# Optimization experiments

Hardware: AMD Instinct MI355X
Metric: run time of the kernel (lower is better)

The kernel has to match this reference:

```python
import jax, jax.numpy as jnp
import numpy as np

NUM_HEADS = 16
HEAD_SIZE = 64
N_EMBD = 1024
BLOCK_SIZE = 2048
BATCH = 2


def setup_inputs() -> dict:
    key = jax.random.key(0)
    ks = jax.random.split(key, 6)
    s = 0.02
    x = jax.random.normal(ks[0], (BATCH, BLOCK_SIZE, N_EMBD), dtype=jnp.float32)
    Wq = jax.random.normal(ks[1], (NUM_HEADS, N_EMBD, HEAD_SIZE), dtype=jnp.float32) * s
    Wk = jax.random.normal(ks[2], (NUM_HEADS, N_EMBD, HEAD_SIZE), dtype=jnp.float32) * s
    Wv = jax.random.normal(ks[3], (NUM_HEADS, N_EMBD, HEAD_SIZE), dtype=jnp.float32) * s
    Wproj = jax.random.normal(ks[4], (NUM_HEADS * HEAD_SIZE, N_EMBD), dtype=jnp.float32) * s
    bproj = jax.random.normal(ks[5], (N_EMBD,), dtype=jnp.float32) * s
    return {"x": x, "Wq": Wq, "Wk": Wk, "Wv": Wv, "Wproj": Wproj, "bproj": bproj}


def reference(x, Wq, Wk, Wv, Wproj, bproj):
    B, S, E = x.shape
    H, _, D = Wq.shape
    # batched per-head projections (equivalent to the per-head Linear loop)
    q = jnp.einsum('bse,hed->bhsd', x, Wq)
    k = jnp.einsum('bse,hed->bhsd', x, Wk)
    v = jnp.einsum('bse,hed->bhsd', x, Wv)
    scale = D ** -0.5
    scores = jnp.einsum('bhqd,bhkd->bhqk', q, k) * scale
    causal = jnp.tril(jnp.ones((S, S), dtype=bool))
    scores = jnp.where(causal, scores, jnp.finfo(scores.dtype).min)
    attn = jax.nn.softmax(scores, axis=-1)
    out = jnp.einsum('bhqk,bhkd->bhqd', attn, v)  # [B,H,S,D]
    out = out.transpose(0, 2, 1, 3).reshape(B, S, H * D)  # concat heads
    return out @ Wproj + bproj
```

## Files before the change

kernel.cpp:

```cpp
#include <hip/hip_runtime.h>
#include <hip/hip_fp16.h>

#define BATCH 2
#define SEQ 2048
#define EMB 1024
#define NH 16
#define HDIM 64

typedef _Float16 h16;
typedef __attribute__((ext_vector_type(8))) _Float16 h8;
typedef __attribute__((ext_vector_type(4))) _Float16 h4;
typedef __attribute__((ext_vector_type(2))) _Float16 h2;
typedef __attribute__((ext_vector_type(4))) float f32x4;

#define MFMA16(a, b, c) __builtin_amdgcn_mfma_f32_16x16x32_f16((a), (b), (c), 0, 0, 0)

__device__ __forceinline__ void g2l16(const void* g, void* l) {
    __builtin_amdgcn_global_load_lds(
        (const __attribute__((address_space(1))) unsigned int*)g,
        (__attribute__((address_space(3))) unsigned int*)l, 16, 0, 0);
}

__global__ __launch_bounds__(256) void k_cast_x(const float* __restrict__ x,
                                                h16* __restrict__ xh) {
    int i = (blockIdx.x * 256 + threadIdx.x) * 4;
    float4 v = *(const float4*)(x + i);
    h4 o = { (h16)v.x, (h16)v.y, (h16)v.z, (h16)v.w };
    *(h4*)(xh + i) = o;
}

__global__ __launch_bounds__(256) void k_tr_qkv3(const float* __restrict__ wq,
                                                 const float* __restrict__ wk,
                                                 const float* __restrict__ wv,
                                                 h16* __restrict__ wcat) {
    __shared__ h16 ld[64][65];
    int g = blockIdx.x >> 4;
    int t = blockIdx.x & 15;
    int h = g / 3, mat = g - h * 3;
    const float* src = (mat == 0) ? wq : (mat == 1) ? wk : wv;
    int e0 = t * 64;
    int c0 = threadIdx.x & 63, r0 = threadIdx.x >> 6;
#pragma unroll
    for (int i = 0; i < 16; i++) {
        int e = i * 4 + r0;
        ld[c0][e] = (h16)src[((size_t)((h << 10) | (e0 + e))) * 64 + c0];
    }
    __syncthreads();
#pragma unroll
    for (int i = 0; i < 16; i++) {
        int d = i * 4 + r0;
        wcat[((size_t)(g * 64 + d) << 10) | (e0 + c0)] = ld[d][c0];
    }
}

__global__ __launch_bounds__(256) void k_tr_wp(const float* __restrict__ w,
                                               h16* __restrict__ wt) {
    __shared__ h16 ld[64][65];
    int kt = blockIdx.x & 15, ntl = blockIdx.x >> 4;
    int c0 = threadIdx.x & 63, r0 = threadIdx.x >> 6;
#pragma unroll
    for (int i = 0; i < 16; i++) {
        int k = i * 4 + r0;
        ld[c0][k] = (h16)w[((size_t)(kt * 64 + k) << 10) | (ntl * 64 + c0)];
    }
    __syncthreads();
#pragma unroll
    for (int i = 0; i < 16; i++) {
        int n = i * 4 + r0;
        wt[((size_t)(ntl * 64 + n) << 10) | (kt * 64 + c0)] = ld[n][c0];
    }
}

__global__ __launch_bounds__(256) void k_qkv(
    const h16* __restrict__ xh, const h16* __restrict__ wcat,
    h16* __restrict__ Q, h16* __restrict__ Kk, h16* __restrict__ Vt) {
    __shared__ h16 As[128 * 64];
    __shared__ h16 Bs[128 * 64];
    int tid = threadIdx.x;
    int wave = tid >> 6, lane = tid & 63;
    int lr = lane & 15, lg = lane >> 4, lx = lr & 7;
    int wr = wave >> 1, wc = wave & 1;
    int swz = (blockIdx.x & 7) * 96 + (blockIdx.x >> 3);
    int nt = swz % 24, mt = swz / 24;

    const char* Ab = (const char*)xh + (size_t)mt * 128 * 2048;
    const char* Bb = (const char*)wcat + (size_t)nt * 128 * 2048;
    int rl = lane >> 3, gc = lane & 7;
    size_t lofs = (size_t)rl * 2048 + ((gc ^ rl) << 4);

    f32x4 acc[4][4];
#pragma unroll
    for (int m = 0; m < 4; m++)
#pragma unroll
        for (int n = 0; n < 4; n++) acc[m][n] = (f32x4){0.f, 0.f, 0.f, 0.f};

    for (int k0 = 0; k0 < 1024; k0 += 64) {
        size_t kb = (size_t)k0 * 2;
#pragma unroll
        for (int c = 0; c < 4; c++) {
            int rb = c * 32 + wave * 8;
            g2l16(Ab + (size_t)rb * 2048 + lofs + kb, As + rb * 64);
            g2l16(Bb + (size_t)rb * 2048 + lofs + kb, Bs + rb * 64);
        }
        __syncthreads();
#pragma unroll
        for (int dc = 0; dc < 2; dc++) {
            h8 a[4], b[4];
#pragma unroll
            for (int m = 0; m < 4; m++)
                a[m] = *(const h8*)&As[(wr * 64 + m * 16 + lr) * 64 + (((dc * 4 + lg) ^ lx) << 3)];
#pragma unroll
            for (int n = 0; n < 4; n++)
                b[n] = *(const h8*)&Bs[(wc * 64 + n * 16 + lr) * 64 + (((dc * 4 + lg) ^ lx) << 3)];
#pragma unroll
            for (int m = 0; m < 4; m++)
#pragma unroll
                for (int n = 0; n < 4; n++)
                    acc[m][n] = MFMA16(a[m], b[n], acc[m][n]);
        }
        __syncthreads();
    }

    int g = nt * 2 + wc;
    int mat = g % 3, hh = g / 3;
    int row0 = mt * 128 + wr * 64;
    if (mat == 2) {
#pragma unroll
        for (int m = 0; m < 4; m++)
#pragma unroll
            for (int n = 0; n < 4; n++) {
                int row = row0 + m * 16 + lg * 4;
                int b = row >> 11, s = row & 2047;
                int bh = b * 16 + hh;
                int d = n * 16 + lr;
                h4 o = { (h16)acc[m][n][0], (h16)acc[m][n][1],
                         (h16)acc[m][n][2], (h16)acc[m][n][3] };
                *(h4*)&Vt[((size_t)bh * 64 + d) * 2048 + s] = o;
            }
    } else {
        h16* dst = mat ? Kk : Q;
        float qs = mat ? 1.0f : 0.18033688011112042f;
#pragma unroll
        for (int m = 0; m < 4; m++)
#pragma unroll
            for (int n = 0; n < 4; n++)
#pragma unroll
                for (int r = 0; r < 4; r++) {
                    int row = row0 + m * 16 + lg * 4 + r;
                    int bh = (row >> 11) * 16 + hh, s = row & 2047;
                    dst[((size_t)bh * 2048 + s) * 64 + n * 16 + lr] =
                        (h16)(acc[m][n][r] * qs);
                }
    }
}

__global__ __launch_bounds__(256) void k_proj(
    const h16* __restrict__ att, const h16* __restrict__ wpt,
    const float* __restrict__ bias, float* __restrict__ out) {
    __shared__ h16 As[128 * 64];
    __shared__ h16 Bs[64 * 64];
    int tid = threadIdx.x;
    int wave = tid >> 6, lane = tid & 63;
    int lr = lane & 15, lg = lane >> 4, lx = lr & 7;
    int swz = (blockIdx.x & 7) * 64 + (blockIdx.x >> 3);
    int nt = swz & 15, mt = swz >> 4;

    const char* Ab = (const char*)att + (size_t)mt * 128 * 2048;
    const char* Bb = (const char*)wpt + (size_t)nt * 64 * 2048;
    int rl = lane >> 3, gc = lane & 7;
    size_t lofs = (size_t)rl * 2048 + ((gc ^ rl) << 4);

    f32x4 acc[2][4];
#pragma unroll
    for (int m = 0; m < 2; m++)
#pragma unroll
        for (int n = 0; n < 4; n++) acc[m][n] = (f32x4){0.f, 0.f, 0.f, 0.f};

    for (int k0 = 0; k0 < 1024; k0 += 64) {
        size_t kb = (size_t)k0 * 2;
#pragma unroll
        for (int c = 0; c < 4; c++) {
            int rb = c * 32 + wave * 8;
            g2l16(Ab + (size_t)rb * 2048 + lofs + kb, As + rb * 64);
            if (c < 2)
                g2l16(Bb + (size_t)rb * 2048 + lofs + kb, Bs + rb * 64);
        }
        __syncthreads();
#pragma unroll
        for (int dc = 0; dc < 2; dc++) {
            h8 a[2], b[4];
#pragma unroll
            for (int m = 0; m < 2; m++)
                a[m] = *(const h8*)&As[(wave * 32 + m * 16 + lr) * 64 + (((dc * 4 + lg) ^ lx) << 3)];
#pragma unroll
            for (int n = 0; n < 4; n++)
                b[n] = *(const h8*)&Bs[(n * 16 + lr) * 64 + (((dc * 4 + lg) ^ lx) << 3)];
#pragma unroll
            for (int m = 0; m < 2; m++)
#pragma unroll
                for (int n = 0; n < 4; n++)
                    acc[m][n] = MFMA16(a[m], b[n], acc[m][n]);
        }
        __syncthreads();
    }

#pragma unroll
    for (int m = 0; m < 2; m++)
#pragma unroll
        for (int n = 0; n < 4; n++)
#pragma unroll
            for (int r = 0; r < 4; r++) {
                int row = mt * 128 + wave * 32 + m * 16 + lg * 4 + r;
                int col = nt * 64 + n * 16 + lr;
                out[(size_t)row * 1024 + col] = acc[m][n][r] + bias[col];
            }
}

__device__ __forceinline__ void stage_kv(h16* Kb, h16* Vb,
                                         const h16* Kp, const h16* Vp,
                                         int ks0, int wave, int lane) {
    int rl = lane >> 3, gc = lane & 7;
    int sg = gc ^ rl;
#pragma unroll
    for (int c8 = 0; c8 < 2; c8++) {
        int rb = wave * 16 + c8 * 8;
        int row = rb + rl;
        g2l16((const char*)Kp + ((size_t)(ks0 + row) << 7) + (sg << 4), Kb + rb * 64);
        g2l16((const char*)Vp + ((size_t)row << 12) + ((size_t)ks0 << 1) + (sg << 4), Vb + rb * 64);
    }
}

__global__ __launch_bounds__(256, 4) void k_attn(
    const h16* __restrict__ Q, const h16* __restrict__ Kk,
    const h16* __restrict__ Vt, h16* __restrict__ att) {
    __shared__ h16 Kb[2][64 * 64];
    __shared__ h16 Vb[2][64 * 64];
    __shared__ h16 lp[4][16][64];

    int i = blockIdx.x;
    int x = i & 7, rest = i >> 3;
    int bh = x + ((rest & 3) << 3);
    int cslot = rest >> 2;
    int c = (cslot < 16) ? cslot : 47 - cslot;
    int b = bh >> 4, h = bh & 15;
    int wave = threadIdx.x >> 6, lane = threadIdx.x & 63;
    int lr = lane & 15, lg = lane >> 4, lx = lr & 7;
    int q0w = c * 64 + wave * 16;

    const h16* Qp = Q + (size_t)bh * SEQ * HDIM;
    const h16* Kp = Kk + (size_t)bh * SEQ * HDIM;
    const h16* Vp = Vt + (size_t)bh * HDIM * SEQ;

    h8 qb[2];
#pragma unroll
    for (int dc = 0; dc < 2; dc++)
        qb[dc] = *(const h8*)(Qp + (size_t)(q0w + lr) * 64 + dc * 32 + lg * 8);

    stage_kv(Kb[0], Vb[0], Kp, Vp, 0, wave, lane);

    float mx = 0.f, lsum = 0.f;
    f32x4 ot[4];
#pragma unroll
    for (int df = 0; df < 4; df++) ot[df] = (f32x4){0.f, 0.f, 0.f, 0.f};

    int nkt = c + 1;
    for (int kt = 0; kt < nkt; ++kt) {
        int ks0 = kt << 6;
        int cur = kt & 1;
        if (kt + 1 < nkt) {
            stage_kv(Kb[cur ^ 1], Vb[cur ^ 1], Kp, Vp, (kt + 1) << 6, wave, lane);
            asm volatile("s_waitcnt vmcnt(4)" ::: "memory");
        } else {
            asm volatile("s_waitcnt vmcnt(0)" ::: "memory");
        }
        __builtin_amdgcn_s_barrier();
        __builtin_amdgcn_sched_barrier(0);
        const h16* Kc = Kb[cur];
        const h16* Vc = Vb[cur];
        f32x4 st[4];
#pragma unroll
        for (int kf = 0; kf < 4; kf++) st[kf] = (f32x4){0.f, 0.f, 0.f, 0.f};
#pragma unroll
        for (int dc = 0; dc < 2; dc++) {
            h8 ka[4];
#pragma unroll
            for (int kf = 0; kf < 4; kf++)
                ka[kf] = *(const h8*)&Kc[(kf * 16 + lr) * 64 + (((dc * 4 + lg) ^ lx) << 3)];
#pragma unroll
            for (int kf = 0; kf < 4; kf++)
                st[kf] = MFMA16(ka[kf], qb[dc], st[kf]);
        }
        h8 va[2][4];
#pragma unroll
        for (int kc = 0; kc < 2; kc++)
#pragma unroll
            for (int df = 0; df < 4; df++)
                va[kc][df] = *(const h8*)&Vc[(df * 16 + lr) * 64 + (((kc * 4 + lg) ^ lx) << 3)];
        if (kt == nkt - 1) {
            int qg = q0w + lr;
#pragma unroll
            for (int kf = 0; kf < 4; kf++)
#pragma unroll
                for (int r = 0; r < 4; r++) {
                    int kg = ks0 + kf * 16 + lg * 4 + r;
                    if (kg > qg) st[kf][r] = -1e30f;
                }
        }
        float tm = st[0][0];
#pragma unroll
        for (int kf = 0; kf < 4; kf++)
#pragma unroll
            for (int r = 0; r < 4; r++) tm = fmaxf(tm, st[kf][r]);
        tm = fmaxf(tm, __shfl_xor(tm, 16));
        tm = fmaxf(tm, __shfl_xor(tm, 32));
        if (__any(tm > mx + 8.f)) {
            float mn = fmaxf(mx, tm);
            float corr = exp2f(mx - mn);
            lsum *= corr;
#pragma unroll
            for (int df = 0; df < 4; df++) ot[df] *= corr;
            mx = mn;
        }
        float ts = 0.f;
#pragma unroll
        for (int kf = 0; kf < 4; kf++) {
            float p0 = exp2f(st[kf][0] - mx);
            float p1 = exp2f(st[kf][1] - mx);
            float p2 = exp2f(st[kf][2] - mx);
            float p3 = exp2f(st[kf][3] - mx);
            ts += (p0 + p1) + (p2 + p3);
            h4 ph = { (h16)p0, (h16)p1, (h16)p2, (h16)p3 };
            *(h4*)&lp[wave][lr][(((kf * 2 + (lg >> 1)) ^ lx) << 3) + ((lg & 1) << 2)] = ph;
        }
        ts += __shfl_xor(ts, 16);
        ts += __shfl_xor(ts, 32);
        lsum += ts;
#pragma unroll
        for (int kc = 0; kc < 2; kc++) {
            h8 pb = *(const h8*)&lp[wave][lr][(((kc * 4 + lg) ^ lx) << 3)];
#pragma unroll
            for (int df = 0; df < 4; df++)
                ot[df] = MFMA16(va[kc][df], pb, ot[df]);
        }
        __builtin_amdgcn_s_barrier();
    }
    float rl2 = 1.f / lsum;
    int q = q0w + lr;
#pragma unroll
    for (int df = 0; df < 4; df++) {
        h4 o = { (h16)(ot[df][0] * rl2), (h16)(ot[df][1] * rl2),
                 (h16)(ot[df][2] * rl2), (h16)(ot[df][3] * rl2) };
        *(h4*)&att[((size_t)(b * SEQ + q)) * 1024 + h * 64 + df * 16 + lg * 4] = o;
    }
}

extern "C" void kernel_launch(void* const* d_in, const int* in_sizes, int n_in,
                              void* d_out, int out_size, void* d_ws, size_t ws_size,
                              hipStream_t stream) {
    const float* x = (const float*)d_in[0];
    const float* Wq = (const float*)d_in[1];
    const float* Wk = (const float*)d_in[2];
    const float* Wv = (const float*)d_in[3];
    const float* Wp = (const float*)d_in[4];
    const float* bp = (const float*)d_in[5];
    float* out = (float*)d_out;

    char* p = (char*)d_ws;
    h16* xh = (h16*)p;   p += (size_t)BATCH * SEQ * EMB * 2;
    h16* wcat = (h16*)p; p += (size_t)NH * 3 * HDIM * EMB * 2;
    h16* wpt = (h16*)p;  p += (size_t)EMB * EMB * 2;
    h16* Qb = (h16*)p;   p += (size_t)BATCH * NH * SEQ * HDIM * 2;
    h16* Kb = (h16*)p;   p += (size_t)BATCH * NH * SEQ * HDIM * 2;
    h16* Vb = (h16*)p;   p += (size_t)BATCH * NH * SEQ * HDIM * 2;
    h16* attb = (h16*)p;

    k_cast_x<<<(BATCH * SEQ * EMB) / 4 / 256, 256, 0, stream>>>(x, xh);
    k_tr_qkv3<<<48 * 16, 256, 0, stream>>>(Wq, Wk, Wv, wcat);
    k_tr_wp<<<16 * 16, 256, 0, stream>>>(Wp, wpt);
    k_qkv<<<32 * 24, 256, 0, stream>>>(xh, wcat, Qb, Kb, Vb);
    k_attn<<<1024, 256, 0, stream>>>(Qb, Kb, Vb, attb);
    k_proj<<<32 * 16, 256, 0, stream>>>(attb, wpt, bp, out);
}
```

Before: 184.7 us.

## Double-buffer GEMM K-tiles and pair causal query tiles per attention block

The QKV and output-projection GEMMs switch to double-buffered K=32 LDS tiles with a new XOR swizzle, so global-to-LDS loads for the next tile overlap the MFMAs on the current one, with one barrier per step. The attention kernel now gives each block a high and a low query tile (31-c and c), halving the grid to 512 blocks. It shares each staged K/V tile between both tiles while they overlap, which balances causal work and reuses K/V loads. The cost is more registers, and the launch bound drops to 2 blocks per SM, which lowers occupancy.

```diff
diff --git a/kernel.cpp b/kernel.cpp
--- a/kernel.cpp
+++ b/kernel.cpp
@@ -1,5 +1,6 @@
 #include <hip/hip_runtime.h>
 #include <hip/hip_fp16.h>
+#include <type_traits>
 
 #define BATCH 2
 #define SEQ 2048
@@ -10,10 +11,10 @@
 typedef _Float16 h16;
 typedef __attribute__((ext_vector_type(8))) _Float16 h8;
 typedef __attribute__((ext_vector_type(4))) _Float16 h4;
-typedef __attribute__((ext_vector_type(2))) _Float16 h2;
 typedef __attribute__((ext_vector_type(4))) float f32x4;
 
 #define MFMA16(a, b, c) __builtin_amdgcn_mfma_f32_16x16x32_f16((a), (b), (c), 0, 0, 0)
+#define VMCNT0() asm volatile("s_waitcnt vmcnt(0)" ::: "memory")
 
 __device__ __forceinline__ void g2l16(const void* g, void* l) {
     __builtin_amdgcn_global_load_lds(
@@ -74,19 +75,30 @@
 __global__ __launch_bounds__(256) void k_qkv(
     const h16* __restrict__ xh, const h16* __restrict__ wcat,
     h16* __restrict__ Q, h16* __restrict__ Kk, h16* __restrict__ Vt) {
-    __shared__ h16 As[128 * 64];
-    __shared__ h16 Bs[128 * 64];
+    __shared__ h16 As[2][128 * 32];
+    __shared__ h16 Bs[2][128 * 32];
     int tid = threadIdx.x;
     int wave = tid >> 6, lane = tid & 63;
-    int lr = lane & 15, lg = lane >> 4, lx = lr & 7;
+    int lr = lane & 15, lg = lane >> 4, l2 = lr & 3;
     int wr = wave >> 1, wc = wave & 1;
     int swz = (blockIdx.x & 7) * 96 + (blockIdx.x >> 3);
     int nt = swz % 24, mt = swz / 24;
 
     const char* Ab = (const char*)xh + (size_t)mt * 128 * 2048;
     const char* Bb = (const char*)wcat + (size_t)nt * 128 * 2048;
-    int rl = lane >> 3, gc = lane & 7;
-    size_t lofs = (size_t)rl * 2048 + ((gc ^ rl) << 4);
+    int rl = lane >> 2, gc = lane & 3;
+
+    auto stage = [&](int buf, int k0) {
+        size_t kb = (size_t)k0 * 2;
+#pragma unroll
+        for (int cc = 0; cc < 2; cc++) {
+            int rb = (wave * 2 + cc) * 16;
+            int row = rb + rl;
+            size_t off = (size_t)row * 2048 + ((size_t)((gc ^ (row & 3)) << 4)) + kb;
+            g2l16(Ab + off, &As[buf][rb * 32]);
+            g2l16(Bb + off, &Bs[buf][rb * 32]);
+        }
+    };
 
     f32x4 acc[4][4];
 #pragma unroll
@@ -94,31 +106,29 @@
 #pragma unroll
         for (int n = 0; n < 4; n++) acc[m][n] = (f32x4){0.f, 0.f, 0.f, 0.f};
 
-    for (int k0 = 0; k0 < 1024; k0 += 64) {
-        size_t kb = (size_t)k0 * 2;
-#pragma unroll
-        for (int c = 0; c < 4; c++) {
-            int rb = c * 32 + wave * 8;
-            g2l16(Ab + (size_t)rb * 2048 + lofs + kb, As + rb * 64);
-            g2l16(Bb + (size_t)rb * 2048 + lofs + kb, Bs + rb * 64);
-        }
-        __syncthreads();
-#pragma unroll
-        for (int dc = 0; dc < 2; dc++) {
-            h8 a[4], b[4];
-#pragma unroll
-            for (int m = 0; m < 4; m++)
-                a[m] = *(const h8*)&As[(wr * 64 + m * 16 + lr) * 64 + (((dc * 4 + lg) ^ lx) << 3)];
+    stage(0, 0);
+    VMCNT0();
+    __builtin_amdgcn_s_barrier();
+    __builtin_amdgcn_sched_barrier(0);
+
+    for (int t = 0; t < 32; ++t) {
+        int cur = t & 1;
+        if (t + 1 < 32) stage(cur ^ 1, (t + 1) * 32);
+        h8 a[4], b[4];
+#pragma unroll
+        for (int m = 0; m < 4; m++)
+            a[m] = *(const h8*)&As[cur][(wr * 64 + m * 16 + lr) * 32 + ((lg ^ l2) << 3)];
+#pragma unroll
+        for (int n = 0; n < 4; n++)
+            b[n] = *(const h8*)&Bs[cur][(wc * 64 + n * 16 + lr) * 32 + ((lg ^ l2) << 3)];
+#pragma unroll
+        for (int m = 0; m < 4; m++)
 #pragma unroll
             for (int n = 0; n < 4; n++)
-                b[n] = *(const h8*)&Bs[(wc * 64 + n * 16 + lr) * 64 + (((dc * 4 + lg) ^ lx) << 3)];
-#pragma unroll
-            for (int m = 0; m < 4; m++)
-#pragma unroll
-                for (int n = 0; n < 4; n++)
-                    acc[m][n] = MFMA16(a[m], b[n], acc[m][n]);
-        }
-        __syncthreads();
+                acc[m][n] = MFMA16(a[m], b[n], acc[m][n]);
+        VMCNT0();
+        __builtin_amdgcn_s_barrier();
+        __builtin_amdgcn_sched_barrier(0);
     }
 
     int g = nt * 2 + wc;
@@ -157,18 +167,32 @@
 __global__ __launch_bounds__(256) void k_proj(
     const h16* __restrict__ att, const h16* __restrict__ wpt,
     const float* __restrict__ bias, float* __restrict__ out) {
-    __shared__ h16 As[128 * 64];
-    __shared__ h16 Bs[64 * 64];
+    __shared__ h16 As[2][128 * 32];
+    __shared__ h16 Bs[2][64 * 32];
     int tid = threadIdx.x;
     int wave = tid >> 6, lane = tid & 63;
-    int lr = lane & 15, lg = lane >> 4, lx = lr & 7;
+    int lr = lane & 15, lg = lane >> 4, l2 = lr & 3;
     int swz = (blockIdx.x & 7) * 64 + (blockIdx.x >> 3);
     int nt = swz & 15, mt = swz >> 4;
 
     const char* Ab = (const char*)att + (size_t)mt * 128 * 2048;
     const char* Bb = (const char*)wpt + (size_t)nt * 64 * 2048;
-    int rl = lane >> 3, gc = lane & 7;
-    size_t lofs = (size_t)rl * 2048 + ((gc ^ rl) << 4);
+    int rl = lane >> 2, gc = lane & 3;
+
+    auto stage = [&](int buf, int k0) {
+        size_t kb = (size_t)k0 * 2;
+#pragma unroll
+        for (int cc = 0; cc < 2; cc++) {
+            int rb = (wave * 2 + cc) * 16;
+            int row = rb + rl;
+            size_t off = (size_t)row * 2048 + ((size_t)((gc ^ (row & 3)) << 4)) + kb;
+            g2l16(Ab + off, &As[buf][rb * 32]);
+        }
+        int rbB = wave * 16;
+        int rowB = rbB + rl;
+        size_t offB = (size_t)rowB * 2048 + ((size_t)((gc ^ (rowB & 3)) << 4)) + kb;
+        g2l16(Bb + offB, &Bs[buf][rbB * 32]);
+    };
 
     f32x4 acc[2][4];
 #pragma unroll
@@ -176,32 +200,29 @@
 #pragma unroll
         for (int n = 0; n < 4; n++) acc[m][n] = (f32x4){0.f, 0.f, 0.f, 0.f};
 
-    for (int k0 = 0; k0 < 1024; k0 += 64) {
-        size_t kb = (size_t)k0 * 2;
-#pragma unroll
-        for (int c = 0; c < 4; c++) {
-            int rb = c * 32 + wave * 8;
-            g2l16(Ab + (size_t)rb * 2048 + lofs + kb, As + rb * 64);
-            if (c < 2)
-                g2l16(Bb + (size_t)rb * 2048 + lofs + kb, Bs + rb * 64);
-        }
-        __syncthreads();
-#pragma unroll
-        for (int dc = 0; dc < 2; dc++) {
-            h8 a[2], b[4];
-#pragma unroll
-            for (int m = 0; m < 2; m++)
-                a[m] = *(const h8*)&As[(wave * 32 + m * 16 + lr) * 64 + (((dc * 4 + lg) ^ lx) << 3)];
+    stage(0, 0);
+    VMCNT0();
+    __builtin_amdgcn_s_barrier();
+    __builtin_amdgcn_sched_barrier(0);
+
+    for (int t = 0; t < 32; ++t) {
+        int cur = t & 1;
+        if (t + 1 < 32) stage(cur ^ 1, (t + 1) * 32);
+        h8 a[2], b[4];
+#pragma unroll
+        for (int m = 0; m < 2; m++)
+            a[m] = *(const h8*)&As[cur][(wave * 32 + m * 16 + lr) * 32 + ((lg ^ l2) << 3)];
+#pragma unroll
+        for (int n = 0; n < 4; n++)
+            b[n] = *(const h8*)&Bs[cur][(n * 16 + lr) * 32 + ((lg ^ l2) << 3)];
+#pragma unroll
+        for (int m = 0; m < 2; m++)
 #pragma unroll
             for (int n = 0; n < 4; n++)
-                b[n] = *(const h8*)&Bs[(n * 16 + lr) * 64 + (((dc * 4 + lg) ^ lx) << 3)];
-#pragma unroll
-            for (int m = 0; m < 2; m++)
-#pragma unroll
-                for (int n = 0; n < 4; n++)
-                    acc[m][n] = MFMA16(a[m], b[n], acc[m][n]);
-        }
-        __syncthreads();
+                acc[m][n] = MFMA16(a[m], b[n], acc[m][n]);
+        VMCNT0();
+        __builtin_amdgcn_s_barrier();
+        __builtin_amdgcn_sched_barrier(0);
     }
 
 #pragma unroll
@@ -230,127 +251,198 @@
     }
 }
 
-__global__ __launch_bounds__(256, 4) void k_attn(
+__global__ __launch_bounds__(256, 2) void k_attn(
     const h16* __restrict__ Q, const h16* __restrict__ Kk,
     const h16* __restrict__ Vt, h16* __restrict__ att) {
     __shared__ h16 Kb[2][64 * 64];
     __shared__ h16 Vb[2][64 * 64];
-    __shared__ h16 lp[4][16][64];
+    __shared__ h16 lp[4][2][16][64];
 
     int i = blockIdx.x;
     int x = i & 7, rest = i >> 3;
     int bh = x + ((rest & 3) << 3);
-    int cslot = rest >> 2;
-    int c = (cslot < 16) ? cslot : 47 - cslot;
+    int c = rest >> 2;
     int b = bh >> 4, h = bh & 15;
     int wave = threadIdx.x >> 6, lane = threadIdx.x & 63;
     int lr = lane & 15, lg = lane >> 4, lx = lr & 7;
-    int q0w = c * 64 + wave * 16;
+    int q0h = (31 - c) * 64 + wave * 16;
+    int q0l = c * 64 + wave * 16;
 
     const h16* Qp = Q + (size_t)bh * SEQ * HDIM;
     const h16* Kp = Kk + (size_t)bh * SEQ * HDIM;
     const h16* Vp = Vt + (size_t)bh * HDIM * SEQ;
 
-    h8 qb[2];
-#pragma unroll
-    for (int dc = 0; dc < 2; dc++)
-        qb[dc] = *(const h8*)(Qp + (size_t)(q0w + lr) * 64 + dc * 32 + lg * 8);
+    h8 qh_[2], ql_[2];
+#pragma unroll
+    for (int dc = 0; dc < 2; dc++) {
+        qh_[dc] = *(const h8*)(Qp + (size_t)(q0h + lr) * 64 + dc * 32 + lg * 8);
+        ql_[dc] = *(const h8*)(Qp + (size_t)(q0l + lr) * 64 + dc * 32 + lg * 8);
+    }
 
     stage_kv(Kb[0], Vb[0], Kp, Vp, 0, wave, lane);
-
-    float mx = 0.f, lsum = 0.f;
-    f32x4 ot[4];
-#pragma unroll
-    for (int df = 0; df < 4; df++) ot[df] = (f32x4){0.f, 0.f, 0.f, 0.f};
-
-    int nkt = c + 1;
+    VMCNT0();
+    __builtin_amdgcn_s_barrier();
+    __builtin_amdgcn_sched_barrier(0);
+
+    float mxh = 0.f, mxl = 0.f, lsh = 0.f, lsl = 0.f;
+    f32x4 oth[4], otl[4];
+#pragma unroll
+    for (int df = 0; df < 4; df++) {
+        oth[df] = (f32x4){0.f, 0.f, 0.f, 0.f};
+        otl[df] = (f32x4){0.f, 0.f, 0.f, 0.f};
+    }
+
+    int nkt = 32 - c;
     for (int kt = 0; kt < nkt; ++kt) {
         int ks0 = kt << 6;
         int cur = kt & 1;
-        if (kt + 1 < nkt) {
+        if (kt + 1 < nkt)
             stage_kv(Kb[cur ^ 1], Vb[cur ^ 1], Kp, Vp, (kt + 1) << 6, wave, lane);
-            asm volatile("s_waitcnt vmcnt(4)" ::: "memory");
-        } else {
-            asm volatile("s_waitcnt vmcnt(0)" ::: "memory");
-        }
+        const h16* Kc = Kb[cur];
+        const h16* Vc = Vb[cur];
+
+        auto body = [&](auto LOC) {
+            constexpr bool LO = decltype(LOC)::value;
+            f32x4 sh[4], sl[4];
+#pragma unroll
+            for (int kf = 0; kf < 4; kf++) {
+                sh[kf] = (f32x4){0.f, 0.f, 0.f, 0.f};
+                sl[kf] = (f32x4){0.f, 0.f, 0.f, 0.f};
+            }
+#pragma unroll
+            for (int dc = 0; dc < 2; dc++) {
+                h8 ka[4];
+#pragma unroll
+                for (int kf = 0; kf < 4; kf++)
+                    ka[kf] = *(const h8*)&Kc[(kf * 16 + lr) * 64 + (((dc * 4 + lg) ^ lx) << 3)];
+#pragma unroll
+                for (int kf = 0; kf < 4; kf++) {
+                    sh[kf] = MFMA16(ka[kf], qh_[dc], sh[kf]);
+                    if constexpr (LO) sl[kf] = MFMA16(ka[kf], ql_[dc], sl[kf]);
+                }
+            }
+            h8 va[2][4];
+#pragma unroll
+            for (int kc = 0; kc < 2; kc++)
+#pragma unroll
+                for (int df = 0; df < 4; df++)
+                    va[kc][df] = *(const h8*)&Vc[(df * 16 + lr) * 64 + (((kc * 4 + lg) ^ lx) << 3)];
+            if (kt == nkt - 1) {
+                int qg = q0h + lr;
+#pragma unroll
+                for (int kf = 0; kf < 4; kf++)
+#pragma unroll
+                    for (int r = 0; r < 4; r++)
+                        if (ks0 + kf * 16 + lg * 4 + r > qg) sh[kf][r] = -1e30f;
+            }
+            if constexpr (LO) {
+                if (kt == c) {
+                    int qg = q0l + lr;
+#pragma unroll
+                    for (int kf = 0; kf < 4; kf++)
+#pragma unroll
+                        for (int r = 0; r < 4; r++)
+                            if (ks0 + kf * 16 + lg * 4 + r > qg) sl[kf][r] = -1e30f;
+                }
+            }
+            float tmh = sh[0][0], tml = 0.f;
+#pragma unroll
+            for (int kf = 0; kf < 4; kf++)
+#pragma unroll
+                for (int r = 0; r < 4; r++) tmh = fmaxf(tmh, sh[kf][r]);
+            tmh = fmaxf(tmh, __shfl_xor(tmh, 16));
+            tmh = fmaxf(tmh, __shfl_xor(tmh, 32));
+            if constexpr (LO) {
+                tml = sl[0][0];
+#pragma unroll
+                for (int kf = 0; kf < 4; kf++)
+#pragma unroll
+                    for (int r = 0; r < 4; r++) tml = fmaxf(tml, sl[kf][r]);
+                tml = fmaxf(tml, __shfl_xor(tml, 16));
+                tml = fmaxf(tml, __shfl_xor(tml, 32));
+            }
+            bool need = (tmh > mxh + 8.f);
+            if constexpr (LO) need = need || (tml > mxl + 8.f);
+            if (__any(need)) {
+                float mn = fmaxf(mxh, tmh);
+                float corr = exp2f(mxh - mn);
+                lsh *= corr;
+#pragma unroll
+                for (int df = 0; df < 4; df++) oth[df] *= corr;
+                mxh = mn;
+                if constexpr (LO) {
+                    float mnl = fmaxf(mxl, tml);
+                    float cl = exp2f(mxl - mnl);
+                    lsl *= cl;
+#pragma unroll
+                    for (int df = 0; df < 4; df++) otl[df] *= cl;
+                    mxl = mnl;
+                }
+            }
+            float tsh = 0.f, tsl = 0.f;
+#pragma unroll
+            for (int kf = 0; kf < 4; kf++) {
+                float a0 = exp2f(sh[kf][0] - mxh), a1 = exp2f(sh[kf][1] - mxh);
+                float a2 = exp2f(sh[kf][2] - mxh), a3 = exp2f(sh[kf][3] - mxh);
+                tsh += (a0 + a1) + (a2 + a3);
+                h4 ph = { (h16)a0, (h16)a1, (h16)a2, (h16)a3 };
+                *(h4*)&lp[wave][0][lr][(((kf * 2 + (lg >> 1)) ^ lx) << 3) + ((lg & 1) << 2)] = ph;
+                if constexpr (LO) {
+                    float b0 = exp2f(sl[kf][0] - mxl), b1 = exp2f(sl[kf][1] - mxl);
+                    float b2 = exp2f(sl[kf][2] - mxl), b3 = exp2f(sl[kf][3] - mxl);
+                    tsl += (b0 + b1) + (b2 + b3);
+                    h4 pl = { (h16)b0, (h16)b1, (h16)b2, (h16)b3 };
+                    *(h4*)&lp[wave][1][lr][(((kf * 2 + (lg >> 1)) ^ lx) << 3) + ((lg & 1) << 2)] = pl;
+                }
+            }
+            tsh += __shfl_xor(tsh, 16);
+            tsh += __shfl_xor(tsh, 32);
+            lsh += tsh;
+            if constexpr (LO) {
+                tsl += __shfl_xor(tsl, 16);
+                tsl += __shfl_xor(tsl, 32);
+                lsl += tsl;
+            }
+#pragma unroll
+            for (int kc = 0; kc < 2; kc++) {
+                h8 pbh = *(const h8*)&lp[wave][0][lr][(((kc * 4 + lg) ^ lx) << 3)];
+#pragma unroll
+                for (int df = 0; df < 4; df++)
+                    oth[df] = MFMA16(va[kc][df], pbh, oth[df]);
+                if constexpr (LO) {
+                    h8 pbl = *(const h8*)&lp[wave][1][lr][(((kc * 4 + lg) ^ lx) << 3)];
+#pragma unroll
+                    for (int df = 0; df < 4; df++)
+                        otl[df] = MFMA16(va[kc][df], pbl, otl[df]);
+                }
+            }
+        };
+        if (kt <= c) body(std::integral_constant<bool, true>{});
+        else         body(std::integral_constant<bool, false>{});
+
+        VMCNT0();
         __builtin_amdgcn_s_barrier();
         __builtin_amdgcn_sched_barrier(0);
-        const h16* Kc = Kb[cur];
-        const h16* Vc = Vb[cur];
-        f32x4 st[4];
-#pragma unroll
-        for (int kf = 0; kf < 4; kf++) st[kf] = (f32x4){0.f, 0.f, 0.f, 0.f};
-#pragma unroll
-        for (int dc = 0; dc < 2; dc++) {
-            h8 ka[4];
-#pragma unroll
-            for (int kf = 0; kf < 4; kf++)
-                ka[kf] = *(const h8*)&Kc[(kf * 16 + lr) * 64 + (((dc * 4 + lg) ^ lx) << 3)];
-#pragma unroll
-            for (int kf = 0; kf < 4; kf++)
-                st[kf] = MFMA16(ka[kf], qb[dc], st[kf]);
+    }
+    {
+        float rl2 = 1.f / lsh;
+        int q = q0h + lr;
+#pragma unroll
+        for (int df = 0; df < 4; df++) {
+            h4 o = { (h16)(oth[df][0] * rl2), (h16)(oth[df][1] * rl2),
+                     (h16)(oth[df][2] * rl2), (h16)(oth[df][3] * rl2) };
+            *(h4*)&att[((size_t)(b * SEQ + q)) * 1024 + h * 64 + df * 16 + lg * 4] = o;
         }
-        h8 va[2][4];
-#pragma unroll
-        for (int kc = 0; kc < 2; kc++)
-#pragma unroll
-            for (int df = 0; df < 4; df++)
-                va[kc][df] = *(const h8*)&Vc[(df * 16 + lr) * 64 + (((kc * 4 + lg) ^ lx) << 3)];
-        if (kt == nkt - 1) {
-            int qg = q0w + lr;
-#pragma unroll
-            for (int kf = 0; kf < 4; kf++)
-#pragma unroll
-                for (int r = 0; r < 4; r++) {
-                    int kg = ks0 + kf * 16 + lg * 4 + r;
-                    if (kg > qg) st[kf][r] = -1e30f;
-                }
+    }
+    {
+        float rl2 = 1.f / lsl;
+        int q = q0l + lr;
+#pragma unroll
+        for (int df = 0; df < 4; df++) {
+            h4 o = { (h16)(otl[df][0] * rl2), (h16)(otl[df][1] * rl2),
+                     (h16)(otl[df][2] * rl2), (h16)(otl[df][3] * rl2) };
+            *(h4*)&att[((size_t)(b * SEQ + q)) * 1024 + h * 64 + df * 16 + lg * 4] = o;
         }
-        float tm = st[0][0];
-#pragma unroll
-        for (int kf = 0; kf < 4; kf++)
-#pragma unroll
-            for (int r = 0; r < 4; r++) tm = fmaxf(tm, st[kf][r]);
-        tm = fmaxf(tm, __shfl_xor(tm, 16));
-        tm = fmaxf(tm, __shfl_xor(tm, 32));
-        if (__any(tm > mx + 8.f)) {
-            float mn = fmaxf(mx, tm);
-            float corr = exp2f(mx - mn);
-            lsum *= corr;
-#pragma unroll
-            for (int df = 0; df < 4; df++) ot[df] *= corr;
-            mx = mn;
-        }
-        float ts = 0.f;
-#pragma unroll
-        for (int kf = 0; kf < 4; kf++) {
-            float p0 = exp2f(st[kf][0] - mx);
-            float p1 = exp2f(st[kf][1] - mx);
-            float p2 = exp2f(st[kf][2] - mx);
-            float p3 = exp2f(st[kf][3] - mx);
-            ts += (p0 + p1) + (p2 + p3);
-            h4 ph = { (h16)p0, (h16)p1, (h16)p2, (h16)p3 };
-            *(h4*)&lp[wave][lr][(((kf * 2 + (lg >> 1)) ^ lx) << 3) + ((lg & 1) << 2)] = ph;
-        }
-        ts += __shfl_xor(ts, 16);
-        ts += __shfl_xor(ts, 32);
-        lsum += ts;
-#pragma unroll
-        for (int kc = 0; kc < 2; kc++) {
-            h8 pb = *(const h8*)&lp[wave][lr][(((kc * 4 + lg) ^ lx) << 3)];
-#pragma unroll
-            for (int df = 0; df < 4; df++)
-                ot[df] = MFMA16(va[kc][df], pb, ot[df]);
-        }
-        __builtin_amdgcn_s_barrier();
-    }
-    float rl2 = 1.f / lsum;
-    int q = q0w + lr;
-#pragma unroll
-    for (int df = 0; df < 4; df++) {
-        h4 o = { (h16)(ot[df][0] * rl2), (h16)(ot[df][1] * rl2),
-                 (h16)(ot[df][2] * rl2), (h16)(ot[df][3] * rl2) };
-        *(h4*)&att[((size_t)(b * SEQ + q)) * 1024 + h * 64 + df * 16 + lg * 4] = o;
     }
 }
 
@@ -378,6 +470,6 @@
     k_tr_qkv3<<<48 * 16, 256, 0, stream>>>(Wq, Wk, Wv, wcat);
     k_tr_wp<<<16 * 16, 256, 0, stream>>>(Wp, wpt);
     k_qkv<<<32 * 24, 256, 0, stream>>>(xh, wcat, Qb, Kb, Vb);
-    k_attn<<<1024, 256, 0, stream>>>(Qb, Kb, Vb, attb);
+    k_attn<<<512, 256, 0, stream>>>(Qb, Kb, Vb, attb);
     k_proj<<<32 * 16, 256, 0, stream>>>(attb, wpt, bp, out);
 }
```

Result: slower. 201.0 us (+8.8%).

## Split long causal attention rows across two blocks and merge partials

Applied to the files above, without the earlier changes.

The attention kernel now splits the key range for query tiles in the second half of the sequence. One block processes keys 0-1023 and another processes the remaining keys, and each writes an fp32 partial output plus its max and sum. The second block also handles a short query tile from the first half. A new merge kernel combines the partial softmax states. The aim is to balance work across blocks for causal attention. The cost is an extra launch, fp32 partial-buffer traffic, and a double-buffer pipeline that now waits with vmcnt(0) on every tile.

```diff
diff --git a/kernel.cpp b/kernel.cpp
--- a/kernel.cpp
+++ b/kernel.cpp
@@ -1,5 +1,6 @@
 #include <hip/hip_runtime.h>
 #include <hip/hip_fp16.h>
+#include <type_traits>
 
 #define BATCH 2
 #define SEQ 2048
@@ -10,10 +11,10 @@
 typedef _Float16 h16;
 typedef __attribute__((ext_vector_type(8))) _Float16 h8;
 typedef __attribute__((ext_vector_type(4))) _Float16 h4;
-typedef __attribute__((ext_vector_type(2))) _Float16 h2;
 typedef __attribute__((ext_vector_type(4))) float f32x4;
 
 #define MFMA16(a, b, c) __builtin_amdgcn_mfma_f32_16x16x32_f16((a), (b), (c), 0, 0, 0)
+#define VMCNT0() asm volatile("s_waitcnt vmcnt(0)" ::: "memory")
 
 __device__ __forceinline__ void g2l16(const void* g, void* l) {
     __builtin_amdgcn_global_load_lds(
@@ -232,7 +233,9 @@
 
 __global__ __launch_bounds__(256, 4) void k_attn(
     const h16* __restrict__ Q, const h16* __restrict__ Kk,
-    const h16* __restrict__ Vt, h16* __restrict__ att) {
+    const h16* __restrict__ Vt, h16* __restrict__ att,
+    float* __restrict__ O1, float* __restrict__ ml1,
+    float* __restrict__ O2, float* __restrict__ ml2) {
     __shared__ h16 Kb[2][64 * 64];
     __shared__ h16 Vb[2][64 * 64];
     __shared__ h16 lp[4][16][64];
@@ -240,118 +243,157 @@
     int i = blockIdx.x;
     int x = i & 7, rest = i >> 3;
     int bh = x + ((rest & 3) << 3);
-    int cslot = rest >> 2;
-    int c = (cslot < 16) ? cslot : 47 - cslot;
+    int c = (rest >> 2) & 15;
+    int half = rest >> 6;
     int b = bh >> 4, h = bh & 15;
     int wave = threadIdx.x >> 6, lane = threadIdx.x & 63;
     int lr = lane & 15, lg = lane >> 4, lx = lr & 7;
-    int q0w = c * 64 + wave * 16;
 
     const h16* Qp = Q + (size_t)bh * SEQ * HDIM;
     const h16* Kp = Kk + (size_t)bh * SEQ * HDIM;
     const h16* Vp = Vt + (size_t)bh * HDIM * SEQ;
 
-    h8 qb[2];
-#pragma unroll
-    for (int dc = 0; dc < 2; dc++)
-        qb[dc] = *(const h8*)(Qp + (size_t)(q0w + lr) * 64 + dc * 32 + lg * 8);
-
-    stage_kv(Kb[0], Vb[0], Kp, Vp, 0, wave, lane);
-
-    float mx = 0.f, lsum = 0.f;
-    f32x4 ot[4];
-#pragma unroll
-    for (int df = 0; df < 4; df++) ot[df] = (f32x4){0.f, 0.f, 0.f, 0.f};
-
-    int nkt = c + 1;
-    for (int kt = 0; kt < nkt; ++kt) {
-        int ks0 = kt << 6;
-        int cur = kt & 1;
-        if (kt + 1 < nkt) {
-            stage_kv(Kb[cur ^ 1], Vb[cur ^ 1], Kp, Vp, (kt + 1) << 6, wave, lane);
-            asm volatile("s_waitcnt vmcnt(4)" ::: "memory");
-        } else {
-            asm volatile("s_waitcnt vmcnt(0)" ::: "memory");
-        }
+    int H = 31 - c;
+
+    auto pass = [&](int q0c, int kt0, int kt1, int diagTile, auto FINALC,
+                    float* Op, float* mlp) {
+        constexpr bool FINAL = decltype(FINALC)::value;
+        int q0 = q0c + wave * 16;
+        h8 qb[2];
+#pragma unroll
+        for (int dc = 0; dc < 2; dc++)
+            qb[dc] = *(const h8*)(Qp + (size_t)(q0 + lr) * 64 + dc * 32 + lg * 8);
+
+        float mx = 0.f, lsum = 0.f;
+        f32x4 ot[4];
+#pragma unroll
+        for (int df = 0; df < 4; df++) ot[df] = (f32x4){0.f, 0.f, 0.f, 0.f};
+
+        stage_kv(Kb[0], Vb[0], Kp, Vp, kt0 << 6, wave, lane);
+        VMCNT0();
         __builtin_amdgcn_s_barrier();
         __builtin_amdgcn_sched_barrier(0);
-        const h16* Kc = Kb[cur];
-        const h16* Vc = Vb[cur];
-        f32x4 st[4];
-#pragma unroll
-        for (int kf = 0; kf < 4; kf++) st[kf] = (f32x4){0.f, 0.f, 0.f, 0.f};
-#pragma unroll
-        for (int dc = 0; dc < 2; dc++) {
-            h8 ka[4];
-#pragma unroll
-            for (int kf = 0; kf < 4; kf++)
-                ka[kf] = *(const h8*)&Kc[(kf * 16 + lr) * 64 + (((dc * 4 + lg) ^ lx) << 3)];
-#pragma unroll
-            for (int kf = 0; kf < 4; kf++)
-                st[kf] = MFMA16(ka[kf], qb[dc], st[kf]);
-        }
-        h8 va[2][4];
-#pragma unroll
-        for (int kc = 0; kc < 2; kc++)
+
+        for (int kt = kt0; kt < kt1; ++kt) {
+            int ks0 = kt << 6;
+            int cur = (kt - kt0) & 1;
+            if (kt + 1 < kt1)
+                stage_kv(Kb[cur ^ 1], Vb[cur ^ 1], Kp, Vp, (kt + 1) << 6, wave, lane);
+            const h16* Kc = Kb[cur];
+            const h16* Vc = Vb[cur];
+            f32x4 st[4];
+#pragma unroll
+            for (int kf = 0; kf < 4; kf++) st[kf] = (f32x4){0.f, 0.f, 0.f, 0.f};
+#pragma unroll
+            for (int dc = 0; dc < 2; dc++) {
+                h8 ka[4];
+#pragma unroll
+                for (int kf = 0; kf < 4; kf++)
+                    ka[kf] = *(const h8*)&Kc[(kf * 16 + lr) * 64 + (((dc * 4 + lg) ^ lx) << 3)];
+#pragma unroll
+                for (int kf = 0; kf < 4; kf++)
+                    st[kf] = MFMA16(ka[kf], qb[dc], st[kf]);
+            }
+            h8 va[2][4];
+#pragma unroll
+            for (int kc = 0; kc < 2; kc++)
+#pragma unroll
+                for (int df = 0; df < 4; df++)
+                    va[kc][df] = *(const h8*)&Vc[(df * 16 + lr) * 64 + (((kc * 4 + lg) ^ lx) << 3)];
+            if (kt == diagTile) {
+                int qg = q0 + lr;
+#pragma unroll
+                for (int kf = 0; kf < 4; kf++)
+#pragma unroll
+                    for (int r = 0; r < 4; r++)
+                        if (ks0 + kf * 16 + lg * 4 + r > qg) st[kf][r] = -1e30f;
+            }
+            float t0 = fmaxf(fmaxf(st[0][0], st[0][1]), fmaxf(st[0][2], st[0][3]));
+            float t1 = fmaxf(fmaxf(st[1][0], st[1][1]), fmaxf(st[1][2], st[1][3]));
+            float t2 = fmaxf(fmaxf(st[2][0], st[2][1]), fmaxf(st[2][2], st[2][3]));
+            float t3 = fmaxf(fmaxf(st[3][0], st[3][1]), fmaxf(st[3][2], st[3][3]));
+            float tm = fmaxf(fmaxf(t0, t1), fmaxf(t2, t3));
+            tm = fmaxf(tm, __shfl_xor(tm, 16));
+            tm = fmaxf(tm, __shfl_xor(tm, 32));
+            if (__any(tm > mx + 8.f)) {
+                float mn = fmaxf(mx, tm);
+                float corr = exp2f(mx - mn);
+                lsum *= corr;
+#pragma unroll
+                for (int df = 0; df < 4; df++) ot[df] *= corr;
+                mx = mn;
+            }
+            float ts = 0.f;
+#pragma unroll
+            for (int kf = 0; kf < 4; kf++) {
+                float p0 = exp2f(st[kf][0] - mx);
+                float p1 = exp2f(st[kf][1] - mx);
+                float p2 = exp2f(st[kf][2] - mx);
+                float p3 = exp2f(st[kf][3] - mx);
+                ts += (p0 + p1) + (p2 + p3);
+                h4 ph = { (h16)p0, (h16)p1, (h16)p2, (h16)p3 };
+                *(h4*)&lp[wave][lr][(((kf * 2 + (lg >> 1)) ^ lx) << 3) + ((lg & 1) << 2)] = ph;
+            }
+            ts += __shfl_xor(ts, 16);
+            ts += __shfl_xor(ts, 32);
+            lsum += ts;
+#pragma unroll
+            for (int kc = 0; kc < 2; kc++) {
+                h8 pb = *(const h8*)&lp[wave][lr][(((kc * 4 + lg) ^ lx) << 3)];
+#pragma unroll
+                for (int df = 0; df < 4; df++)
+                    ot[df] = MFMA16(va[kc][df], pb, ot[df]);
+            }
+            VMCNT0();
+            __builtin_amdgcn_s_barrier();
+            __builtin_amdgcn_sched_barrier(0);
+        }
+        int q = q0 + lr;
+        if constexpr (FINAL) {
+            float rl2 = 1.f / lsum;
+#pragma unroll
+            for (int df = 0; df < 4; df++) {
+                h4 o = { (h16)(ot[df][0] * rl2), (h16)(ot[df][1] * rl2),
+                         (h16)(ot[df][2] * rl2), (h16)(ot[df][3] * rl2) };
+                *(h4*)&att[((size_t)(b * SEQ + q)) * 1024 + h * 64 + df * 16 + lg * 4] = o;
+            }
+        } else {
+            size_t r = ((size_t)bh << 10) + (q - 1024);
+            float* Ob = Op + r * 64;
 #pragma unroll
             for (int df = 0; df < 4; df++)
-                va[kc][df] = *(const h8*)&Vc[(df * 16 + lr) * 64 + (((kc * 4 + lg) ^ lx) << 3)];
-        if (kt == nkt - 1) {
-            int qg = q0w + lr;
-#pragma unroll
-            for (int kf = 0; kf < 4; kf++)
-#pragma unroll
-                for (int r = 0; r < 4; r++) {
-                    int kg = ks0 + kf * 16 + lg * 4 + r;
-                    if (kg > qg) st[kf][r] = -1e30f;
-                }
-        }
-        float tm = st[0][0];
-#pragma unroll
-        for (int kf = 0; kf < 4; kf++)
-#pragma unroll
-            for (int r = 0; r < 4; r++) tm = fmaxf(tm, st[kf][r]);
-        tm = fmaxf(tm, __shfl_xor(tm, 16));
-        tm = fmaxf(tm, __shfl_xor(tm, 32));
-        if (__any(tm > mx + 8.f)) {
-            float mn = fmaxf(mx, tm);
-            float corr = exp2f(mx - mn);
-            lsum *= corr;
-#pragma unroll
-            for (int df = 0; df < 4; df++) ot[df] *= corr;
-            mx = mn;
-        }
-        float ts = 0.f;
-#pragma unroll
-        for (int kf = 0; kf < 4; kf++) {
-            float p0 = exp2f(st[kf][0] - mx);
-            float p1 = exp2f(st[kf][1] - mx);
-            float p2 = exp2f(st[kf][2] - mx);
-            float p3 = exp2f(st[kf][3] - mx);
-            ts += (p0 + p1) + (p2 + p3);
-            h4 ph = { (h16)p0, (h16)p1, (h16)p2, (h16)p3 };
-            *(h4*)&lp[wave][lr][(((kf * 2 + (lg >> 1)) ^ lx) << 3) + ((lg & 1) << 2)] = ph;
-        }
-        ts += __shfl_xor(ts, 16);
-        ts += __shfl_xor(ts, 32);
-        lsum += ts;
-#pragma unroll
-        for (int kc = 0; kc < 2; kc++) {
-            h8 pb = *(const h8*)&lp[wave][lr][(((kc * 4 + lg) ^ lx) << 3)];
-#pragma unroll
-            for (int df = 0; df < 4; df++)
-                ot[df] = MFMA16(va[kc][df], pb, ot[df]);
-        }
-        __builtin_amdgcn_s_barrier();
-    }
-    float rl2 = 1.f / lsum;
-    int q = q0w + lr;
-#pragma unroll
-    for (int df = 0; df < 4; df++) {
-        h4 o = { (h16)(ot[df][0] * rl2), (h16)(ot[df][1] * rl2),
-                 (h16)(ot[df][2] * rl2), (h16)(ot[df][3] * rl2) };
-        *(h4*)&att[((size_t)(b * SEQ + q)) * 1024 + h * 64 + df * 16 + lg * 4] = o;
-    }
+                *(f32x4*)&Ob[df * 16 + lg * 4] = ot[df];
+            if (lg == 0) {
+                mlp[r * 2] = mx;
+                mlp[r * 2 + 1] = lsum;
+            }
+        }
+    };
+
+    if (half == 0) {
+        pass(H * 64, 0, 16, H, std::integral_constant<bool, false>{}, O1, ml1);
+    } else {
+        pass(H * 64, 16, H + 1, H, std::integral_constant<bool, false>{}, O2, ml2);
+        pass(c * 64, 0, c + 1, c, std::integral_constant<bool, true>{}, nullptr, nullptr);
+    }
+}
+
+__global__ __launch_bounds__(256) void k_merge(
+    const float* __restrict__ O1, const float* __restrict__ ml1,
+    const float* __restrict__ O2, const float* __restrict__ ml2,
+    h16* __restrict__ att) {
+    int t = blockIdx.x * 256 + threadIdx.x;
+    int d = t & 63;
+    int r = t >> 6;
+    int bh = r >> 10, qh = r & 1023;
+    float m1 = ml1[r * 2], l1 = ml1[r * 2 + 1];
+    float m2 = ml2[r * 2], l2 = ml2[r * 2 + 1];
+    float m = fmaxf(m1, m2);
+    float w1 = exp2f(m1 - m), w2 = exp2f(m2 - m);
+    float o = w1 * O1[t] + w2 * O2[t];
+    float l = w1 * l1 + w2 * l2;
+    int b = bh >> 4, h = bh & 15;
+    att[((size_t)(b * SEQ + 1024 + qh)) * 1024 + h * 64 + d] = (h16)(o / l);
 }
 
 extern "C" void kernel_launch(void* const* d_in, const int* in_sizes, int n_in,
@@ -372,12 +414,17 @@
     h16* Qb = (h16*)p;   p += (size_t)BATCH * NH * SEQ * HDIM * 2;
     h16* Kb = (h16*)p;   p += (size_t)BATCH * NH * SEQ * HDIM * 2;
     h16* Vb = (h16*)p;   p += (size_t)BATCH * NH * SEQ * HDIM * 2;
-    h16* attb = (h16*)p;
+    h16* attb = (h16*)p; p += (size_t)BATCH * SEQ * EMB * 2;
+    float* O1 = (float*)p;  p += (size_t)32 * 1024 * 64 * 4;
+    float* O2 = (float*)p;  p += (size_t)32 * 1024 * 64 * 4;
+    float* ml1 = (float*)p; p += (size_t)32 * 1024 * 2 * 4;
+    float* ml2 = (float*)p;
 
     k_cast_x<<<(BATCH * SEQ * EMB) / 4 / 256, 256, 0, stream>>>(x, xh);
     k_tr_qkv3<<<48 * 16, 256, 0, stream>>>(Wq, Wk, Wv, wcat);
     k_tr_wp<<<16 * 16, 256, 0, stream>>>(Wp, wpt);
     k_qkv<<<32 * 24, 256, 0, stream>>>(xh, wcat, Qb, Kb, Vb);
-    k_attn<<<1024, 256, 0, stream>>>(Qb, Kb, Vb, attb);
+    k_attn<<<1024, 256, 0, stream>>>(Qb, Kb, Vb, attb, O1, ml1, O2, ml2);
+    k_merge<<<(32 * 1024 * 64) / 256, 256, 0, stream>>>(O1, ml1, O2, ml2, attb);
     k_proj<<<32 * 16, 256, 0, stream>>>(attb, wpt, bp, out);
 }
```

Result: slower. 196.7 us (+6.5%).
